# Kernel tuning notes

Hardware: AMD Instinct MI355X
Metric: run time of the kernel (lower is better)

The kernel has to match this reference:

```python
import jax, jax.numpy as jnp
import numpy as np
import math

DIM = 768
EDGE_DIM = 2
NUM_HEADS = 12
MAX_LEN = 257
B, N = 2, 256
HEAD_DIM = DIM // NUM_HEADS
SCALE = HEAD_DIM ** (-0.5)
NEG = -2.0 ** 15


def _sinusoidal_pe(max_len, hid):
    position = np.arange(max_len, dtype=np.float32)[:, None]
    div_term = np.exp(np.arange(0, hid, 2, dtype=np.float32) * (-math.log(10000.0) / hid))
    pe = np.zeros((max_len, hid), dtype=np.float32)
    pe[:, 0::2] = np.sin(position * div_term)
    pe[:, 1::2] = np.cos(position * div_term)
    return jnp.asarray(pe)


def setup_inputs() -> dict:
    key = jax.random.key(0)
    ks = jax.random.split(key, 8)
    std = DIM ** (-0.5)
    return {
        "x": jax.random.normal(ks[0], (B, N, DIM), jnp.float32),
        "edges": jax.random.randint(ks[1], (B, N, N, EDGE_DIM), 0, MAX_LEN),
        "mask": jnp.ones((B, N, N), dtype=bool),
        "pe": _sinusoidal_pe(MAX_LEN, DIM),
        "qkv_w": jax.random.normal(ks[2], (3 * DIM, DIM), jnp.float32) * std,
        "e_w1": jax.random.normal(ks[3], (DIM, EDGE_DIM * DIM), jnp.float32) * std,
        "e_b1": jnp.zeros((DIM,), jnp.float32),
        "e_w2": jax.random.normal(ks[4], (NUM_HEADS, DIM), jnp.float32) * std,
        "e_b2": jnp.zeros((NUM_HEADS,), jnp.float32),
        "out_w": jax.random.normal(ks[5], (DIM, DIM), jnp.float32) * std,
        "out_b": jnp.zeros((DIM,), jnp.float32),
    }


def reference(x, edges, mask, pe, qkv_w, e_w1, e_b1, e_w2, e_b2, out_w, out_b):
    b, n, c = x.shape
    # edge embedding: (B,N,N,2) -> (B,N,N,2,C) -> (B,N,N,2C)
    e = pe[edges].reshape(b, n, n, EDGE_DIM * c)
    # proj_e: Linear -> ReLU -> Linear => (B,N,N,h)
    e = jax.nn.relu(jnp.einsum('bnmf,df->bnmd', e, e_w1) + e_b1)
    e = jnp.einsum('bnmd,hd->bnmh', e, e_w2) + e_b2
    # qkv
    qkv = (x @ qkv_w.T).reshape(b, n, 3, NUM_HEADS, HEAD_DIM)
    q, k, v = qkv[:, :, 0], qkv[:, :, 1], qkv[:, :, 2]  # (B,N,H,D)
    attn = jnp.einsum('bnhd,bmhd->bhnm', q, k) * SCALE + e.transpose(0, 3, 1, 2)
    attn = jnp.where(mask[:, None], attn, NEG)
    attn = jax.nn.softmax(attn, axis=-1)
    out = jnp.einsum('bhnm,bmhd->bnhd', attn, v).reshape(b, n, c)
    out = out @ out_w.T + out_b
    return out, e
```

## Files before the change

kernel.cpp:

```cpp
#include <hip/hip_runtime.h>
#include <hip/hip_bf16.h>
#include <math.h>

#define SCALE 0.125f
typedef float f32x4 __attribute__((ext_vector_type(4)));
typedef short bf16x8 __attribute__((ext_vector_type(8)));
typedef unsigned short u16;

#define OFF_TT   0
#define OFF_QKVB 197376
#define OFF_O1B  787200
#define OFF_PT   983808

__device__ __forceinline__ u16 f2bfbits(float x) {
    return __builtin_bit_cast(u16, __float2bfloat16(x));
}
__device__ __forceinline__ float bf2f(short b) {
    return __builtin_bit_cast(float, (unsigned)((u16)b) << 16);
}

__device__ __forceinline__ bf16x8 ld8(const void* base, size_t off, int fp32) {
    if (fp32) {
        const float* p = (const float*)base + off;
        float4 v0 = *(const float4*)p;
        float4 v1 = *(const float4*)(p + 4);
        bf16x8 r;
        r[0] = (short)f2bfbits(v0.x); r[1] = (short)f2bfbits(v0.y);
        r[2] = (short)f2bfbits(v0.z); r[3] = (short)f2bfbits(v0.w);
        r[4] = (short)f2bfbits(v1.x); r[5] = (short)f2bfbits(v1.y);
        r[6] = (short)f2bfbits(v1.z); r[7] = (short)f2bfbits(v1.w);
        return r;
    }
    return *(const bf16x8*)((const u16*)base + off);
}

__device__ __forceinline__ void gemm_core(
    const void* A, int afp, const void* B, int bfp, int bmode,
    const float* bias, int bias_n, void* C, int ldc,
    int M, int N, int K, int cbf16, int row0, int col0,
    u16* As, u16* Bs)
{
    const int tid = threadIdx.x, lane = tid & 63, wv = tid >> 6;
    const int lr = tid >> 3, ls = tid & 7;

    const int ar0 = min(row0 + lr, M - 1), ar1 = min(row0 + lr + 32, M - 1);
    const int bj0 = col0 + lr, bj1 = col0 + lr + 32;
    const size_t aoff0 = (size_t)ar0 * K;
    const size_t aoff1 = (size_t)ar1 * K;
    const size_t boff0 = bmode ? (size_t)(bj0 % 768) * 1536 + (size_t)(bj0 / 768) * 768
                               : (size_t)bj0 * K;
    const size_t boff1 = bmode ? (size_t)(bj1 % 768) * 1536 + (size_t)(bj1 / 768) * 768
                               : (size_t)bj1 * K;

    const int swzl = (lr & 7) << 4;
    char* wA0 = (char*)As + lr * 128 + ((ls * 16) ^ swzl);
    char* wA1 = (char*)As + (lr + 32) * 128 + ((ls * 16) ^ swzl);
    char* wB0 = (char*)Bs + lr * 128 + ((ls * 16) ^ swzl);
    char* wB1 = (char*)Bs + (lr + 32) * 128 + ((ls * 16) ^ swzl);

    const int c = lane & 15, kg = lane >> 4;
    const int arow = wv * 16 + c;
    const int rsw = (c & 7) << 4;

    f32x4 acc[4] = {{0.f,0.f,0.f,0.f},{0.f,0.f,0.f,0.f},
                    {0.f,0.f,0.f,0.f},{0.f,0.f,0.f,0.f}};
    bf16x8 pa0, pa1, pb0, pb1;

    const int nt = K >> 6;
    pa0 = ld8(A, aoff0 + ls * 8, afp);
    pa1 = ld8(A, aoff1 + ls * 8, afp);
    pb0 = ld8(B, boff0 + ls * 8, bfp);
    pb1 = ld8(B, boff1 + ls * 8, bfp);

    for (int t = 0; t < nt; ++t) {
        *(bf16x8*)wA0 = pa0; *(bf16x8*)wA1 = pa1;
        *(bf16x8*)wB0 = pb0; *(bf16x8*)wB1 = pb1;
        if (t + 1 < nt) {
            const int ko = (t + 1) * 64 + ls * 8;
            pa0 = ld8(A, aoff0 + ko, afp);
            pa1 = ld8(A, aoff1 + ko, afp);
            pb0 = ld8(B, boff0 + ko, bfp);
            pb1 = ld8(B, boff1 + ko, bfp);
        }
        __syncthreads();
        #pragma unroll
        for (int kc = 0; kc < 2; ++kc) {
            bf16x8 af = *(const bf16x8*)((char*)As + arow * 128 +
                                         ((kc * 64 + kg * 16) ^ rsw));
            #pragma unroll
            for (int nn = 0; nn < 4; ++nn) {
                bf16x8 bf = *(const bf16x8*)((char*)Bs + (nn * 16 + c) * 128 +
                                             ((kc * 64 + kg * 16) ^ rsw));
                acc[nn] = __builtin_amdgcn_mfma_f32_16x16x32_bf16(af, bf, acc[nn], 0, 0, 0);
            }
        }
        __syncthreads();
    }

    #pragma unroll
    for (int nn = 0; nn < 4; ++nn) {
        const int gc = col0 + nn * 16 + c;
        const float bv = (bias && gc < bias_n) ? bias[gc] : 0.f;
        #pragma unroll
        for (int r = 0; r < 4; ++r) {
            const int gr = row0 + wv * 16 + kg * 4 + r;
            if (gr < M) {
                float v = acc[nn][r] + bv;
                if (cbf16) ((u16*)C)[(size_t)gr * ldc + gc] = f2bfbits(v);
                else       ((float*)C)[(size_t)gr * ldc + gc] = v;
            }
        }
    }
}

__global__ __launch_bounds__(256) void gemm2_kernel(
    const float* pe, const float* e_w1, const float* e_b1, u16* ttb,
    const float* x, const float* qkv_w, u16* qkvb)
{
    __shared__ u16 As[64 * 64];
    __shared__ u16 Bs[64 * 64];
    const int bid = blockIdx.x;
    if (bid < 120) {
        gemm_core(pe, 1, e_w1, 1, 1, e_b1, 768, ttb, 1536,
                  257, 1536, 768, 1, (bid / 24) * 64, (bid % 24) * 64, As, Bs);
    } else {
        const int b2 = bid - 120;
        gemm_core(x, 1, qkv_w, 1, 0, nullptr, 0, qkvb, 2304,
                  512, 2304, 768, 1, (b2 / 36) * 64, (b2 % 36) * 64, As, Bs);
    }
}

__global__ __launch_bounds__(256) void pair_kernel(
    const u16* __restrict__ TTB, const float* __restrict__ w2,
    const float* __restrict__ b2, float* __restrict__ PT)
{
    __shared__ u16 TBs[16 * 776];
    __shared__ u16 W2s[12 * 776];
    const int tid = threadIdx.x, lane = tid & 63, wv = tid >> 6;

    #pragma unroll
    for (int it = 0; it < 11; ++it) {
        const int seg = it * 256 + tid;
        if (seg < 1536) {
            const int row = seg / 96, s = seg % 96;
            int grow = row < 8 ? (int)blockIdx.y * 8 + row
                               : (int)blockIdx.x * 8 + (row - 8);
            grow = min(grow, 256);
            const int gcol = (row < 8 ? 0 : 768) + s * 8;
            *(bf16x8*)(TBs + row * 776 + s * 8) =
                *(const bf16x8*)(TTB + (size_t)grow * 1536 + gcol);
        } else if (seg < 2688) {
            const int s2 = seg - 1536;
            const int row = s2 / 96, s = s2 % 96;
            *(bf16x8*)(W2s + row * 776 + s * 8) =
                ld8(w2, (size_t)row * 768 + s * 8, 1);
        }
    }
    __syncthreads();

    const int c = lane & 15, kg = lane >> 4;
    const int p0l = 2 * wv + (c >> 3);
    const int p1l = c & 7;
    const int hcl = c < 12 ? c : 0;
    const u16* wr = W2s + hcl * 776;
    const u16* r0 = TBs + p0l * 776;
    const u16* r1 = TBs + (8 + p1l) * 776;

    f32x4 accA = {0.f, 0.f, 0.f, 0.f};
    f32x4 accB = {0.f, 0.f, 0.f, 0.f};
    #pragma unroll 4
    for (int kc2 = 0; kc2 < 12; ++kc2) {
        const int koA = kc2 * 64 + kg * 8;
        const int koB = koA + 32;
        bf16x8 a0A = *(const bf16x8*)(r0 + koA);
        bf16x8 a1A = *(const bf16x8*)(r1 + koA);
        bf16x8 a0B = *(const bf16x8*)(r0 + koB);
        bf16x8 a1B = *(const bf16x8*)(r1 + koB);
        bf16x8 afA, afB;
        #pragma unroll
        for (int j = 0; j < 8; ++j) {
            afA[j] = (short)f2bfbits(fmaxf(bf2f(a0A[j]) + bf2f(a1A[j]), 0.f));
            afB[j] = (short)f2bfbits(fmaxf(bf2f(a0B[j]) + bf2f(a1B[j]), 0.f));
        }
        bf16x8 bfA = *(const bf16x8*)(wr + koA);
        bf16x8 bfB = *(const bf16x8*)(wr + koB);
        accA = __builtin_amdgcn_mfma_f32_16x16x32_bf16(afA, bfA, accA, 0, 0, 0);
        accB = __builtin_amdgcn_mfma_f32_16x16x32_bf16(afB, bfB, accB, 0, 0, 0);
    }
    f32x4 acc = accA + accB;

    #pragma unroll
    for (int r = 0; r < 4; ++r) {
        const int P = kg * 4 + r;
        const int p0 = blockIdx.y * 8 + 2 * wv + (P >> 3);
        const int p1 = blockIdx.x * 8 + (P & 7);
        if (c < 12 && p0 < 257 && p1 < 257)
            PT[((size_t)p0 * 257 + p1) * 12 + c] = acc[r] + b2[c];
    }
}

__global__ __launch_bounds__(128) void attn_kernel(
    const u16* __restrict__ qkvb, const int* __restrict__ edges,
    const float* __restrict__ PT, u16* __restrict__ o1b)
{
    __shared__ u16 P[32 * 256];
    __shared__ u16 Vt[64 * 256];
    const int tid = threadIdx.x, lane = tid & 63, wv = tid >> 6;
    const int qt = blockIdx.x, h = blockIdx.y, b = blockIdx.z;
    const int n0 = qt * 32;
    const u16* qb = qkvb + (size_t)b * 256 * 2304 + h * 64;
    const u16* kb = qb + 768;
    const u16* vb = qb + 1536;

    #pragma unroll
    for (int half = 0; half < 2; ++half) {
        const int m = tid + half * 128;
        const u16* vrow = vb + (size_t)m * 2304;
        const int m2 = m * 2;
        #pragma unroll
        for (int dc = 0; dc < 8; ++dc) {
            bf16x8 vv = *(const bf16x8*)(vrow + dc * 8);
            #pragma unroll
            for (int j = 0; j < 8; ++j) {
                const int d = dc * 8 + j;
                *(u16*)((char*)Vt + d * 512 + (m2 ^ ((d & 7) << 4))) = (u16)vv[j];
            }
        }
    }

    const int c = lane & 15, kg = lane >> 4;

    const u16* qrow = qb + (size_t)(n0 + wv * 16 + c) * 2304;
    bf16x8 qf0 = *(const bf16x8*)(qrow + kg * 8);
    bf16x8 qf1 = *(const bf16x8*)(qrow + 32 + kg * 8);

    f32x4 s[16];
    #pragma unroll
    for (int t = 0; t < 16; ++t) {
        const u16* krow = kb + (size_t)(t * 16 + c) * 2304;
        bf16x8 kf0 = *(const bf16x8*)(krow + kg * 8);
        bf16x8 kf1 = *(const bf16x8*)(krow + 32 + kg * 8);
        f32x4 a = {0.f, 0.f, 0.f, 0.f};
        a = __builtin_amdgcn_mfma_f32_16x16x32_bf16(qf0, kf0, a, 0, 0, 0);
        a = __builtin_amdgcn_mfma_f32_16x16x32_bf16(qf1, kf1, a, 0, 0, 0);
        s[t] = a;
    }

    #pragma unroll
    for (int r = 0; r < 4; ++r) {
        const int n = n0 + wv * 16 + kg * 4 + r;
        const int2* er = (const int2*)(edges + 2 * (((size_t)b * 256 + n) << 8));
        #pragma unroll
        for (int t = 0; t < 16; ++t) {
            const int2 pp = er[t * 16 + c];
            const float ev = PT[((size_t)pp.x * 257 + pp.y) * 12 + h];
            s[t][r] = fmaf(s[t][r], SCALE, ev);
        }
    }

    float inv[4];
    #pragma unroll
    for (int r = 0; r < 4; ++r) {
        float mx = s[0][r];
        #pragma unroll
        for (int t = 1; t < 16; ++t) mx = fmaxf(mx, s[t][r]);
        #pragma unroll
        for (int off = 1; off < 16; off <<= 1) mx = fmaxf(mx, __shfl_xor(mx, off));
        float sum = 0.f;
        #pragma unroll
        for (int t = 0; t < 16; ++t) { s[t][r] = __expf(s[t][r] - mx); sum += s[t][r]; }
        #pragma unroll
        for (int off = 1; off < 16; off <<= 1) sum += __shfl_xor(sum, off);
        inv[r] = 1.f / sum;
    }

    #pragma unroll
    for (int r = 0; r < 4; ++r) {
        const int n = wv * 16 + kg * 4 + r;
        char* prow = (char*)P + n * 512;
        const int nsw = (n & 7) << 4;
        #pragma unroll
        for (int t = 0; t < 16; ++t)
            *(u16*)(prow + (((t * 16 + c) * 2) ^ nsw)) = f2bfbits(s[t][r] * inv[r]);
    }
    __syncthreads();

    const int rsw = (c & 7) << 4;
    f32x4 o[4] = {{0.f,0.f,0.f,0.f},{0.f,0.f,0.f,0.f},
                  {0.f,0.f,0.f,0.f},{0.f,0.f,0.f,0.f}};
    #pragma unroll
    for (int mc = 0; mc < 8; ++mc) {
        bf16x8 pf = *(const bf16x8*)((char*)P + (wv * 16 + c) * 512 +
                                     ((mc * 64 + kg * 16) ^ rsw));
        #pragma unroll
        for (int dt = 0; dt < 4; ++dt) {
            bf16x8 vf = *(const bf16x8*)((char*)Vt + (dt * 16 + c) * 512 +
                                         ((mc * 64 + kg * 16) ^ rsw));
            o[dt] = __builtin_amdgcn_mfma_f32_16x16x32_bf16(pf, vf, o[dt], 0, 0, 0);
        }
    }

    #pragma unroll
    for (int dt = 0; dt < 4; ++dt)
        #pragma unroll
        for (int r = 0; r < 4; ++r) {
            const int gn = b * 256 + n0 + wv * 16 + kg * 4 + r;
            o1b[(size_t)gn * 768 + h * 64 + dt * 16 + c] = f2bfbits(o[dt][r]);
        }
}

__global__ __launch_bounds__(256) void proj_lookup_kernel(
    const u16* __restrict__ o1b, const float* __restrict__ out_w,
    const float* __restrict__ out_b, float* __restrict__ out,
    const int* __restrict__ edges, const float* __restrict__ PT,
    float* __restrict__ e_out)
{
    __shared__ u16 As[64 * 64];
    __shared__ u16 Bs[64 * 64];
    const int bid = blockIdx.x;
    if (bid >= 96) {
        const int idx = (bid - 96) * 256 + threadIdx.x;
        const int2 pp = *(const int2*)(edges + 2 * idx);
        const float4* src = (const float4*)(PT + ((size_t)pp.x * 257 + pp.y) * 12);
        float4 v0 = src[0], v1 = src[1], v2 = src[2];
        float4* eo = (float4*)(e_out + (size_t)idx * 12);
        eo[0] = v0; eo[1] = v1; eo[2] = v2;
        return;
    }
    gemm_core(o1b, 0, out_w, 1, 0, out_b, 1 << 30, out, 768,
              512, 768, 768, 0, (bid / 12) * 64, (bid % 12) * 64, As, Bs);
}

extern "C" void kernel_launch(void* const* d_in, const int* in_sizes, int n_in,
                              void* d_out, int out_size, void* d_ws, size_t ws_size,
                              hipStream_t stream)
{
    const float* x     = (const float*)d_in[0];
    const int*   edges = (const int*)d_in[1];
    const float* pe    = (const float*)d_in[3];
    const float* qkv_w = (const float*)d_in[4];
    const float* e_w1  = (const float*)d_in[5];
    const float* e_b1  = (const float*)d_in[6];
    const float* e_w2  = (const float*)d_in[7];
    const float* e_b2  = (const float*)d_in[8];
    const float* out_w = (const float*)d_in[9];
    const float* out_b = (const float*)d_in[10];

    float* out   = (float*)d_out;
    float* e_out = out + 2 * 256 * 768;

    float* ws   = (float*)d_ws;
    u16*   ttb  = (u16*)(ws + OFF_TT);
    u16*   qkvb = (u16*)(ws + OFF_QKVB);
    u16*   o1b  = (u16*)(ws + OFF_O1B);
    float* PT   = ws + OFF_PT;

    gemm2_kernel<<<408, 256, 0, stream>>>(pe, e_w1, e_b1, ttb, x, qkv_w, qkvb);
    pair_kernel<<<dim3(33, 33), 256, 0, stream>>>(ttb, e_w2, e_b2, PT);
    attn_kernel<<<dim3(8, 12, 2), 128, 0, stream>>>(qkvb, edges, PT, o1b);
    proj_lookup_kernel<<<608, 256, 0, stream>>>(o1b, out_w, out_b, out,
                                                edges, PT, e_out);
}
```

Measured before the change: 62.68 us.

## Replace LDS-tiled GEMM core with direct global-to-register MFMA loads

The shared-memory staged GEMM (swizzled LDS tiles, register prefetch, two barriers per k-tile) is replaced by a version where each lane loads its MFMA A and B fragments straight from global memory, converting fp32 to bf16 in registers. This removes the LDS traffic and __syncthreads, and the shared allocations in the GEMM kernels. In exchange, each wave re-reads B columns that other waves also read and A is shared across four nn loads only, so global and L2 traffic rises and the loads are strided per lane rather than coalesced.

```diff
diff --git a/kernel.cpp b/kernel.cpp
--- a/kernel.cpp
+++ b/kernel.cpp
@@ -34,67 +34,41 @@
     return *(const bf16x8*)((const u16*)base + off);
 }
 
-__device__ __forceinline__ void gemm_core(
+__device__ __forceinline__ void gemm_direct(
     const void* A, int afp, const void* B, int bfp, int bmode,
     const float* bias, int bias_n, void* C, int ldc,
-    int M, int N, int K, int cbf16, int row0, int col0,
-    u16* As, u16* Bs)
+    int M, int N, int K, int cbf16, int row0, int col0)
 {
     const int tid = threadIdx.x, lane = tid & 63, wv = tid >> 6;
-    const int lr = tid >> 3, ls = tid & 7;
-
-    const int ar0 = min(row0 + lr, M - 1), ar1 = min(row0 + lr + 32, M - 1);
-    const int bj0 = col0 + lr, bj1 = col0 + lr + 32;
-    const size_t aoff0 = (size_t)ar0 * K;
-    const size_t aoff1 = (size_t)ar1 * K;
-    const size_t boff0 = bmode ? (size_t)(bj0 % 768) * 1536 + (size_t)(bj0 / 768) * 768
-                               : (size_t)bj0 * K;
-    const size_t boff1 = bmode ? (size_t)(bj1 % 768) * 1536 + (size_t)(bj1 / 768) * 768
-                               : (size_t)bj1 * K;
-
-    const int swzl = (lr & 7) << 4;
-    char* wA0 = (char*)As + lr * 128 + ((ls * 16) ^ swzl);
-    char* wA1 = (char*)As + (lr + 32) * 128 + ((ls * 16) ^ swzl);
-    char* wB0 = (char*)Bs + lr * 128 + ((ls * 16) ^ swzl);
-    char* wB1 = (char*)Bs + (lr + 32) * 128 + ((ls * 16) ^ swzl);
-
     const int c = lane & 15, kg = lane >> 4;
-    const int arow = wv * 16 + c;
-    const int rsw = (c & 7) << 4;
+
+    const int arow = min(row0 + wv * 16 + c, M - 1);
+    const char* abase = afp ? (const char*)((const float*)A + (size_t)arow * K)
+                            : (const char*)((const u16*)A + (size_t)arow * K);
+
+    const char* bbase[4];
+    #pragma unroll
+    for (int nn = 0; nn < 4; ++nn) {
+        const int j = col0 + nn * 16 + c;
+        const size_t boff = bmode ? (size_t)(j % 768) * 1536 + (size_t)(j / 768) * 768
+                                  : (size_t)j * K;
+        bbase[nn] = bfp ? (const char*)((const float*)B + boff)
+                        : (const char*)((const u16*)B + boff);
+    }
 
     f32x4 acc[4] = {{0.f,0.f,0.f,0.f},{0.f,0.f,0.f,0.f},
                     {0.f,0.f,0.f,0.f},{0.f,0.f,0.f,0.f}};
-    bf16x8 pa0, pa1, pb0, pb1;
-
-    const int nt = K >> 6;
-    pa0 = ld8(A, aoff0 + ls * 8, afp);
-    pa1 = ld8(A, aoff1 + ls * 8, afp);
-    pb0 = ld8(B, boff0 + ls * 8, bfp);
-    pb1 = ld8(B, boff1 + ls * 8, bfp);
-
-    for (int t = 0; t < nt; ++t) {
-        *(bf16x8*)wA0 = pa0; *(bf16x8*)wA1 = pa1;
-        *(bf16x8*)wB0 = pb0; *(bf16x8*)wB1 = pb1;
-        if (t + 1 < nt) {
-            const int ko = (t + 1) * 64 + ls * 8;
-            pa0 = ld8(A, aoff0 + ko, afp);
-            pa1 = ld8(A, aoff1 + ko, afp);
-            pb0 = ld8(B, boff0 + ko, bfp);
-            pb1 = ld8(B, boff1 + ko, bfp);
-        }
-        __syncthreads();
-        #pragma unroll
-        for (int kc = 0; kc < 2; ++kc) {
-            bf16x8 af = *(const bf16x8*)((char*)As + arow * 128 +
-                                         ((kc * 64 + kg * 16) ^ rsw));
-            #pragma unroll
-            for (int nn = 0; nn < 4; ++nn) {
-                bf16x8 bf = *(const bf16x8*)((char*)Bs + (nn * 16 + c) * 128 +
-                                             ((kc * 64 + kg * 16) ^ rsw));
-                acc[nn] = __builtin_amdgcn_mfma_f32_16x16x32_bf16(af, bf, acc[nn], 0, 0, 0);
-            }
-        }
-        __syncthreads();
+
+    const int nkc = K >> 5;
+    #pragma unroll 4
+    for (int kc = 0; kc < nkc; ++kc) {
+        const int ko = kc * 32 + kg * 8;
+        bf16x8 af = ld8(abase, ko, afp);
+        #pragma unroll
+        for (int nn = 0; nn < 4; ++nn) {
+            bf16x8 bf = ld8(bbase[nn], ko, bfp);
+            acc[nn] = __builtin_amdgcn_mfma_f32_16x16x32_bf16(af, bf, acc[nn], 0, 0, 0);
+        }
     }
 
     #pragma unroll
@@ -117,16 +91,14 @@
     const float* pe, const float* e_w1, const float* e_b1, u16* ttb,
     const float* x, const float* qkv_w, u16* qkvb)
 {
-    __shared__ u16 As[64 * 64];
-    __shared__ u16 Bs[64 * 64];
     const int bid = blockIdx.x;
     if (bid < 120) {
-        gemm_core(pe, 1, e_w1, 1, 1, e_b1, 768, ttb, 1536,
-                  257, 1536, 768, 1, (bid / 24) * 64, (bid % 24) * 64, As, Bs);
+        gemm_direct(pe, 1, e_w1, 1, 1, e_b1, 768, ttb, 1536,
+                    257, 1536, 768, 1, (bid / 24) * 64, (bid % 24) * 64);
     } else {
         const int b2 = bid - 120;
-        gemm_core(x, 1, qkv_w, 1, 0, nullptr, 0, qkvb, 2304,
-                  512, 2304, 768, 1, (b2 / 36) * 64, (b2 % 36) * 64, As, Bs);
+        gemm_direct(x, 1, qkv_w, 1, 0, nullptr, 0, qkvb, 2304,
+                    512, 2304, 768, 1, (b2 / 36) * 64, (b2 % 36) * 64);
     }
 }
 
@@ -315,8 +287,6 @@
     const int* __restrict__ edges, const float* __restrict__ PT,
     float* __restrict__ e_out)
 {
-    __shared__ u16 As[64 * 64];
-    __shared__ u16 Bs[64 * 64];
     const int bid = blockIdx.x;
     if (bid >= 96) {
         const int idx = (bid - 96) * 256 + threadIdx.x;
@@ -327,8 +297,8 @@
         eo[0] = v0; eo[1] = v1; eo[2] = v2;
         return;
     }
-    gemm_core(o1b, 0, out_w, 1, 0, out_b, 1 << 30, out, 768,
-              512, 768, 768, 0, (bid / 12) * 64, (bid % 12) * 64, As, Bs);
+    gemm_direct(o1b, 0, out_w, 1, 0, out_b, 1 << 30, out, 768,
+                512, 768, 768, 0, (bid / 12) * 64, (bid % 12) * 64);
 }
 
 extern "C" void kernel_launch(void* const* d_in, const int* in_sizes, int n_in,
```

New measurement: 124.0 us. +97.8%, slower.

## Double-buffer LDS tiles in projection GEMMs and remap blocks for XCD locality

Applied to the files above, without the earlier changes.

Adds a double-buffered GEMM core that prefetches the next K-tile from global memory into registers while computing on the current LDS buffer, with one barrier per K-step. It also remaps block IDs so that blocks sharing the same B columns land on the same XCD, aiming for better L2 reuse. The change doubles shared memory per block and raises register pressure, which may reduce occupancy.

```diff
diff --git a/kernel.cpp b/kernel.cpp
--- a/kernel.cpp
+++ b/kernel.cpp
@@ -34,6 +34,102 @@
     return *(const bf16x8*)((const u16*)base + off);
 }
 
+__device__ __forceinline__ void gemm_db(
+    const void* A, int afp, const void* B, int bfp, int bmode,
+    const float* bias, int bias_n, void* C, int ldc,
+    int M, int N, int K, int cbf16, int row0, int col0,
+    u16* As, u16* Bs)
+{
+    const int tid = threadIdx.x, lane = tid & 63, wv = tid >> 6;
+    const int lr = tid >> 3, ls = tid & 7;
+
+    const int ar0 = min(row0 + lr, M - 1), ar1 = min(row0 + lr + 32, M - 1);
+    const int bj0 = col0 + lr, bj1 = col0 + lr + 32;
+    const size_t aoff0 = (size_t)ar0 * K;
+    const size_t aoff1 = (size_t)ar1 * K;
+    const size_t boff0 = bmode ? (size_t)(bj0 % 768) * 1536 + (size_t)(bj0 / 768) * 768
+                               : (size_t)bj0 * K;
+    const size_t boff1 = bmode ? (size_t)(bj1 % 768) * 1536 + (size_t)(bj1 / 768) * 768
+                               : (size_t)bj1 * K;
+
+    const int swzl = (lr & 7) << 4;
+    const int w0o = lr * 128 + ((ls * 16) ^ swzl);
+    const int w1o = (lr + 32) * 128 + ((ls * 16) ^ swzl);
+
+    const int c = lane & 15, kg = lane >> 4;
+    const int arow = wv * 16 + c;
+    const int rsw = (c & 7) << 4;
+
+    f32x4 acc[4] = {{0.f,0.f,0.f,0.f},{0.f,0.f,0.f,0.f},
+                    {0.f,0.f,0.f,0.f},{0.f,0.f,0.f,0.f}};
+    bf16x8 pa0, pa1, pb0, pb1;
+
+    const int nt = K >> 6;
+
+    pa0 = ld8(A, aoff0 + ls * 8, afp);
+    pa1 = ld8(A, aoff1 + ls * 8, afp);
+    pb0 = ld8(B, boff0 + ls * 8, bfp);
+    pb1 = ld8(B, boff1 + ls * 8, bfp);
+    *(bf16x8*)((char*)As + w0o) = pa0; *(bf16x8*)((char*)As + w1o) = pa1;
+    *(bf16x8*)((char*)Bs + w0o) = pb0; *(bf16x8*)((char*)Bs + w1o) = pb1;
+    if (nt > 1) {
+        const int ko = 64 + ls * 8;
+        pa0 = ld8(A, aoff0 + ko, afp);
+        pa1 = ld8(A, aoff1 + ko, afp);
+        pb0 = ld8(B, boff0 + ko, bfp);
+        pb1 = ld8(B, boff1 + ko, bfp);
+    }
+    __syncthreads();
+
+    for (int t = 0; t < nt; ++t) {
+        const int rb = (t & 1) << 13;
+        #pragma unroll
+        for (int kc = 0; kc < 2; ++kc) {
+            bf16x8 af = *(const bf16x8*)((char*)As + rb + arow * 128 +
+                                         ((kc * 64 + kg * 16) ^ rsw));
+            #pragma unroll
+            for (int nn = 0; nn < 4; ++nn) {
+                bf16x8 bf = *(const bf16x8*)((char*)Bs + rb + (nn * 16 + c) * 128 +
+                                             ((kc * 64 + kg * 16) ^ rsw));
+                acc[nn] = __builtin_amdgcn_mfma_f32_16x16x32_bf16(af, bf, acc[nn], 0, 0, 0);
+            }
+        }
+        if (t + 1 < nt) {
+            bf16x8 na0, na1, nb0, nb1;
+            const bool have = (t + 2 < nt);
+            if (have) {
+                const int ko = (t + 2) * 64 + ls * 8;
+                na0 = ld8(A, aoff0 + ko, afp);
+                na1 = ld8(A, aoff1 + ko, afp);
+                nb0 = ld8(B, boff0 + ko, bfp);
+                nb1 = ld8(B, boff1 + ko, bfp);
+            }
+            const int wb = ((t + 1) & 1) << 13;
+            *(bf16x8*)((char*)As + wb + w0o) = pa0;
+            *(bf16x8*)((char*)As + wb + w1o) = pa1;
+            *(bf16x8*)((char*)Bs + wb + w0o) = pb0;
+            *(bf16x8*)((char*)Bs + wb + w1o) = pb1;
+            if (have) { pa0 = na0; pa1 = na1; pb0 = nb0; pb1 = nb1; }
+        }
+        __syncthreads();
+    }
+
+    #pragma unroll
+    for (int nn = 0; nn < 4; ++nn) {
+        const int gc = col0 + nn * 16 + c;
+        const float bv = (bias && gc < bias_n) ? bias[gc] : 0.f;
+        #pragma unroll
+        for (int r = 0; r < 4; ++r) {
+            const int gr = row0 + wv * 16 + kg * 4 + r;
+            if (gr < M) {
+                float v = acc[nn][r] + bv;
+                if (cbf16) ((u16*)C)[(size_t)gr * ldc + gc] = f2bfbits(v);
+                else       ((float*)C)[(size_t)gr * ldc + gc] = v;
+            }
+        }
+    }
+}
+
 __device__ __forceinline__ void gemm_core(
     const void* A, int afp, const void* B, int bfp, int bmode,
     const float* bias, int bias_n, void* C, int ldc,
@@ -117,16 +213,20 @@
     const float* pe, const float* e_w1, const float* e_b1, u16* ttb,
     const float* x, const float* qkv_w, u16* qkvb)
 {
-    __shared__ u16 As[64 * 64];
-    __shared__ u16 Bs[64 * 64];
+    __shared__ u16 As[2 * 64 * 64];
+    __shared__ u16 Bs[2 * 64 * 64];
     const int bid = blockIdx.x;
     if (bid < 120) {
-        gemm_core(pe, 1, e_w1, 1, 1, e_b1, 768, ttb, 1536,
-                  257, 1536, 768, 1, (bid / 24) * 64, (bid % 24) * 64, As, Bs);
+        const int sb = (bid % 8) * 15 + bid / 8;
+        const int col = sb / 5, row = sb % 5;
+        gemm_db(pe, 1, e_w1, 1, 1, e_b1, 768, ttb, 1536,
+                257, 1536, 768, 1, row * 64, col * 64, As, Bs);
     } else {
         const int b2 = bid - 120;
-        gemm_core(x, 1, qkv_w, 1, 0, nullptr, 0, qkvb, 2304,
-                  512, 2304, 768, 1, (b2 / 36) * 64, (b2 % 36) * 64, As, Bs);
+        const int sb = (b2 % 8) * 36 + b2 / 8;
+        const int col = sb / 8, row = sb % 8;
+        gemm_db(x, 1, qkv_w, 1, 0, nullptr, 0, qkvb, 2304,
+                512, 2304, 768, 1, row * 64, col * 64, As, Bs);
     }
 }
 
```

Result: faster. 60.64 us (median of 3 runs) (-3.3%).
